# Kernel tuning notes

Measured on AMD Instinct MI355X. Metric: run time of the kernel, lower is better.

Reference implementation:

```python
import jax, jax.numpy as jnp
import numpy as np

N = 20000        # total atoms (atomic environments)
NFEAT = 2784     # power-spectrum feature size: sum_l n_max[l]^2 * n_pseudo^2
P = 4            # n_pseudo (alchemical pseudo-species)
H = 256          # MLP hidden width
S = 500          # number of structures
NSPEC = 8        # number of chemical species (len(all_species))
AVG_ATOMS = N / S  # average_number_of_atoms used for energy normalization


def setup_inputs() -> dict:
    key = jax.random.key(0)
    ks = jax.random.split(key, 8)
    features = jax.random.normal(ks[0], (N, NFEAT), dtype=jnp.float32)
    species = jax.random.randint(ks[1], (N,), 0, NSPEC)
    structure_idx = jax.random.randint(ks[2], (N,), 0, S)
    # combination matrix: Linear(n_species -> n_pseudo), no bias
    W_comb = jax.random.normal(ks[3], (NSPEC, P), dtype=jnp.float32) / np.float32(np.sqrt(NSPEC))
    # per-pseudo-species MLP weights (bias=False throughout)
    W1 = jax.random.normal(ks[4], (P, NFEAT, H), dtype=jnp.float32) / np.float32(np.sqrt(NFEAT))
    W2 = jax.random.normal(ks[5], (P, H, H), dtype=jnp.float32) / np.float32(np.sqrt(H))
    W3 = jax.random.normal(ks[6], (P, H, H), dtype=jnp.float32) / np.float32(np.sqrt(H))
    W4 = jax.random.normal(ks[7], (P, H, 1), dtype=jnp.float32) / np.float32(np.sqrt(H))
    return {"features": features, "W_comb": W_comb, "W1": W1, "W2": W2,
            "W3": W3, "W4": W4, "species": species, "structure_idx": structure_idx}


def reference(features, W_comb, W1, W2, W3, W4, species, structure_idx):
    # one-hot species encoding followed by combination_matrix linear map.
    # one_hot(species) @ W_comb  ==  W_comb[species]  (gather form, no [N, NSPEC] matmul)
    pseudo_w = W_comb[species]                                   # [N, P]
    # outer-product feature embedding: features[:, :, None] * pseudo_w[:, None, :]
    emb = features[:, :, None] * pseudo_w[:, None, :]            # [N, NFEAT, P]
    # per-pseudo-species MLP (Linear no-bias -> SiLU) x3 -> Linear to scalar,
    # vectorized over the pseudo dimension instead of a Python loop.
    h = jax.nn.silu(jnp.einsum('nfp,pfh->nph', emb, W1))         # [N, P, H]
    h = jax.nn.silu(jnp.einsum('nph,phk->npk', h, W2))           # [N, P, H]
    h = jax.nn.silu(jnp.einsum('nph,phk->npk', h, W3))           # [N, P, H]
    per_pseudo_e = jnp.einsum('nph,pho->npo', h, W4)[..., 0]     # [N, P]
    atomic_energies = per_pseudo_e.sum(axis=1) / np.float32(np.sqrt(P))  # [N]
    # scatter-add atomic energies into per-structure energies (index_add_)
    energies = jax.ops.segment_sum(atomic_energies, structure_idx, num_segments=S)
    return energies / np.float32(AVG_ATOMS)                     # [S]
```

## Files before the change

kernel.cpp:

```cpp
#include <hip/hip_runtime.h>
#include <hip/hip_bf16.h>
#include <stdint.h>

#define N_ATOMS 20000
#define NFEAT   2784
#define KP1     2816
#define KT1     44
#define SS      500
#define NPAD    20224
#define MCOLS   1024

typedef __attribute__((ext_vector_type(8))) short s16x8;
typedef __attribute__((ext_vector_type(4))) float f32x4;

static __device__ __forceinline__ unsigned short f2b(float f) {
    __hip_bfloat16 h = __float2bfloat16(f);
    return __builtin_bit_cast(unsigned short, h);
}
static __device__ __forceinline__ float b2f(unsigned short u) {
    unsigned int x = ((unsigned int)u) << 16;
    return __builtin_bit_cast(float, x);
}

#define GLOAD16(g, l) __builtin_amdgcn_global_load_lds( \
    (const __attribute__((address_space(1))) void*)(g), \
    (__attribute__((address_space(3))) void*)(l), 16, 0, 0)

__global__ void conv_feat(const float* __restrict__ F, unsigned short* __restrict__ out) {
    int row = blockIdx.x;
    int t = threadIdx.x;
    const float4* src = (const float4*)(F + (size_t)row * NFEAT);
    unsigned short* dst = out + (size_t)row * KP1;
    for (int g = t; g < KP1 / 4; g += 256) {
        float4 v;
        if (g < NFEAT / 4) v = src[g];
        else { v.x = 0.f; v.y = 0.f; v.z = 0.f; v.w = 0.f; }
        ushort4 o;
        o.x = f2b(v.x); o.y = f2b(v.y); o.z = f2b(v.z); o.w = f2b(v.w);
        *(ushort4*)(dst + g * 4) = o;
    }
}

__global__ void pack_w(const float* __restrict__ W, unsigned short* __restrict__ Bt,
                       int KD, int KP) {
    __shared__ unsigned short tile[32][256];
    int p = blockIdx.y;
    int f0 = blockIdx.x * 32;
    int t = threadIdx.x;
    #pragma unroll 4
    for (int i = 0; i < 32; ++i) {
        int f = f0 + i;
        float v = (f < KD) ? W[((size_t)p * KD + f) * 256 + t] : 0.f;
        tile[i][t] = f2b(v);
    }
    __syncthreads();
    unsigned short* drow = Bt + (size_t)(p * 256 + t) * KP + f0;
    #pragma unroll
    for (int i = 0; i < 32; i += 4) {
        ushort4 o;
        o.x = tile[i][t]; o.y = tile[i + 1][t]; o.z = tile[i + 2][t]; o.w = tile[i + 3][t];
        *(ushort4*)(drow + i) = o;
    }
}

__global__ void prep_small(const float* __restrict__ W2, const float* __restrict__ W3,
                           unsigned short* __restrict__ B2t, unsigned short* __restrict__ B3t,
                           const float* __restrict__ Wc, const int* __restrict__ spec,
                           float* __restrict__ pw, float* __restrict__ out) {
    __shared__ unsigned short tile[32][256];
    int b = blockIdx.x;
    int t = threadIdx.x;
    if (b < 64) {
        const float* W = (b < 32) ? W2 : W3;
        unsigned short* Bt = (b < 32) ? B2t : B3t;
        int bb = b & 31;
        int p = bb >> 3;
        int f0 = (bb & 7) * 32;
        #pragma unroll 4
        for (int i = 0; i < 32; ++i) {
            int f = f0 + i;
            tile[i][t] = f2b(W[((size_t)p * 256 + f) * 256 + t]);
        }
        __syncthreads();
        unsigned short* drow = Bt + (size_t)(p * 256 + t) * 256 + f0;
        #pragma unroll
        for (int i = 0; i < 32; i += 4) {
            ushort4 o;
            o.x = tile[i][t]; o.y = tile[i + 1][t]; o.z = tile[i + 2][t]; o.w = tile[i + 3][t];
            *(ushort4*)(drow + i) = o;
        }
    } else if (b < 143) {
        int n = (b - 64) * 256 + t;
        if (n < N_ATOMS) {
            int s = spec[n];
            float4 v = *(const float4*)(Wc + s * 4);
            *(float4*)(pw + n * 4) = v;
        }
    } else {
        for (int i = t; i < SS; i += 256) out[i] = 0.f;
    }
}

__global__ __launch_bounds__(512, 4) void gemm1_pipe(
    const unsigned short* __restrict__ A,
    const unsigned short* __restrict__ Bt,
    const float* __restrict__ pw,
    unsigned short* __restrict__ C)
{
    __shared__ __align__(16) unsigned short lds_a[2 * 8192];
    __shared__ __align__(16) unsigned short lds_b[2 * 8192];

    int bid = blockIdx.x;
    int swz = (bid & 7) * 158 + (bid >> 3);
    int rowTile = swz >> 3;
    int colTile = swz & 7;
    int rowBase = rowTile * 128;
    int colBase = colTile * 128;
    int p = colTile >> 1;

    int t0 = threadIdx.x;
    int wave = t0 >> 6;
    int lane = t0 & 63;
    int wm = wave >> 1;
    int wn = wave & 1;

    int rA = t0 >> 3;
    int ckl = ((t0 & 7) ^ (rA & 7)) << 3;
    const unsigned short* sa = A + (size_t)(rowBase + rA) * KP1 + ckl;
    const unsigned short* sb = Bt + (size_t)(colBase + rA) * KP1 + ckl;

    int ra0 = wm * 32 + (lane & 15);
    int rb0 = wn * 64 + (lane & 15);
    int xr = lane & 7;
    int c0 = lane >> 4;

    f32x4 acc[2][4];
    f32x4 z4 = {0.f, 0.f, 0.f, 0.f};
    #pragma unroll
    for (int i = 0; i < 2; ++i)
        #pragma unroll
        for (int j = 0; j < 4; ++j) acc[i][j] = z4;

#define STAGE1(SB) do { \
    GLOAD16(sa,                     lds_a + (SB) * 8192 + t0 * 8); \
    GLOAD16(sa + (size_t)64 * KP1,  lds_a + (SB) * 8192 + 4096 + t0 * 8); \
    GLOAD16(sb,                     lds_b + (SB) * 8192 + t0 * 8); \
    GLOAD16(sb + (size_t)64 * KP1,  lds_b + (SB) * 8192 + 4096 + t0 * 8); \
    sa += 64; sb += 64; \
} while (0)

    STAGE1(0);
    STAGE1(1);
    asm volatile("s_waitcnt vmcnt(4)" ::: "memory");
    __builtin_amdgcn_s_barrier();
    __builtin_amdgcn_sched_barrier(0);

#define FSTEP(CB) do { \
    s16x8 af[2][2], bv[2][4]; \
    _Pragma("unroll") \
    for (int kk = 0; kk < 2; ++kk) { \
        int ch = ((((kk << 2) | c0) ^ xr) << 3); \
        _Pragma("unroll") \
        for (int fm = 0; fm < 2; ++fm) \
            af[kk][fm] = *(const s16x8*)&lds_a[(CB) * 8192 + (ra0 + fm * 16) * 64 + ch]; \
        _Pragma("unroll") \
        for (int fn = 0; fn < 4; ++fn) \
            bv[kk][fn] = *(const s16x8*)&lds_b[(CB) * 8192 + (rb0 + fn * 16) * 64 + ch]; \
    } \
    asm volatile("s_waitcnt lgkmcnt(0)" ::: "memory"); \
    __builtin_amdgcn_sched_barrier(0); \
    __builtin_amdgcn_s_barrier();             \
    __builtin_amdgcn_sched_barrier(0); \
    STAGE1(CB);                               \
    __builtin_amdgcn_s_setprio(1); \
    _Pragma("unroll") \
    for (int kk = 0; kk < 2; ++kk) \
        _Pragma("unroll") \
        for (int fm = 0; fm < 2; ++fm) \
            _Pragma("unroll") \
            for (int fn = 0; fn < 4; ++fn) \
                acc[fm][fn] = __builtin_amdgcn_mfma_f32_16x16x32_bf16( \
                    af[kk][fm], bv[kk][fn], acc[fm][fn], 0, 0, 0); \
    __builtin_amdgcn_s_setprio(0); \
    asm volatile("s_waitcnt vmcnt(4)" ::: "memory");    \
    __builtin_amdgcn_s_barrier(); \
    __builtin_amdgcn_sched_barrier(0); \
} while (0)

#define TSTEP(CB, DRAIN) do { \
    s16x8 af[2][2], bv[2][4]; \
    _Pragma("unroll") \
    for (int kk = 0; kk < 2; ++kk) { \
        int ch = ((((kk << 2) | c0) ^ xr) << 3); \
        _Pragma("unroll") \
        for (int fm = 0; fm < 2; ++fm) \
            af[kk][fm] = *(const s16x8*)&lds_a[(CB) * 8192 + (ra0 + fm * 16) * 64 + ch]; \
        _Pragma("unroll") \
        for (int fn = 0; fn < 4; ++fn) \
            bv[kk][fn] = *(const s16x8*)&lds_b[(CB) * 8192 + (rb0 + fn * 16) * 64 + ch]; \
    } \
    _Pragma("unroll") \
    for (int kk = 0; kk < 2; ++kk) \
        _Pragma("unroll") \
        for (int fm = 0; fm < 2; ++fm) \
            _Pragma("unroll") \
            for (int fn = 0; fn < 4; ++fn) \
                acc[fm][fn] = __builtin_amdgcn_mfma_f32_16x16x32_bf16( \
                    af[kk][fm], bv[kk][fn], acc[fm][fn], 0, 0, 0); \
    if (DRAIN) { \
        asm volatile("s_waitcnt vmcnt(0)" ::: "memory"); \
        __builtin_amdgcn_s_barrier(); \
        __builtin_amdgcn_sched_barrier(0); \
    } \
} while (0)

    for (int it = 0; it < 21; ++it) {
        FSTEP(0);
        FSTEP(1);
    }
    TSTEP(0, 1);
    TSTEP(1, 0);
#undef FSTEP
#undef TSTEP
#undef STAGE1

    int rGrp = (lane >> 4) << 2;
    int cLane = lane & 15;
    #pragma unroll
    for (int fm = 0; fm < 2; ++fm) {
        int r0 = rowBase + wm * 32 + fm * 16 + rGrp;
        float pwv[4];
        #pragma unroll
        for (int j = 0; j < 4; ++j) pwv[j] = pw[(size_t)(r0 + j) * 4 + p];
        #pragma unroll
        for (int fn = 0; fn < 4; ++fn) {
            int c = colBase + wn * 64 + fn * 16 + cLane;
            f32x4 a = acc[fm][fn];
            #pragma unroll
            for (int j = 0; j < 4; ++j) {
                float x = a[j] * pwv[j];
                float s = x / (1.f + __expf(-x));
                C[(size_t)(r0 + j) * MCOLS + c] = f2b(s);
            }
        }
    }
}

template<int USE_PW>
__global__ __launch_bounds__(256, 2) void gemm_silu(
    const unsigned short* __restrict__ A, int lda,
    const unsigned short* __restrict__ Bt, int ldb,
    int K, int aOffPerP,
    const float* __restrict__ pw,
    unsigned short* __restrict__ C)
{
    __shared__ __align__(16) unsigned short lds_a[128 * 64];
    __shared__ __align__(16) unsigned short lds_b[128 * 64];

    int bid = blockIdx.x;
    int colTile = bid & 7;
    int rowTile = bid >> 3;
    int rowBase = rowTile * 128;
    int colBase = colTile * 128;
    int p = colBase >> 8;
    int aOff = p * aOffPerP;

    int t = threadIdx.x;
    int wave = t >> 6;
    int lane = t & 63;
    int wm = wave >> 1, wn = wave & 1;

    int trow = t >> 3;
    int kcol = (((t & 7) ^ (trow & 7)) << 3);
    const unsigned short* srcA = A + (size_t)(rowBase + trow) * lda + aOff + kcol;
    const unsigned short* srcB = Bt + (size_t)(colBase + trow) * ldb + kcol;

    f32x4 acc[4][4];
    f32x4 z4 = {0.f, 0.f, 0.f, 0.f};
    #pragma unroll
    for (int i = 0; i < 4; ++i)
        #pragma unroll
        for (int j = 0; j < 4; ++j) acc[i][j] = z4;

    int rb = wm * 64 + (lane & 15);
    int cb = wn * 64 + (lane & 15);
    int c0 = lane >> 4;
    int xr = lane & 7;

    int KT = K >> 6;
    for (int kt = 0; kt < KT; ++kt) {
        #pragma unroll
        for (int i = 0; i < 4; ++i) {
            GLOAD16(srcA + (size_t)i * 32 * lda, lds_a + i * 2048 + wave * 512);
            GLOAD16(srcB + (size_t)i * 32 * ldb, lds_b + i * 2048 + wave * 512);
        }
        srcA += 64; srcB += 64;
        __syncthreads();

        #pragma unroll
        for (int kk = 0; kk < 2; ++kk) {
            s16x8 af[4], bfr[4];
            int ch = (((kk << 2) | c0) ^ xr) << 3;
            #pragma unroll
            for (int fm = 0; fm < 4; ++fm)
                af[fm] = *(const s16x8*)&lds_a[(rb + fm * 16) * 64 + ch];
            #pragma unroll
            for (int fn = 0; fn < 4; ++fn)
                bfr[fn] = *(const s16x8*)&lds_b[(cb + fn * 16) * 64 + ch];
            #pragma unroll
            for (int fm = 0; fm < 4; ++fm)
                #pragma unroll
                for (int fn = 0; fn < 4; ++fn)
                    acc[fm][fn] = __builtin_amdgcn_mfma_f32_16x16x32_bf16(
                        af[fm], bfr[fn], acc[fm][fn], 0, 0, 0);
        }
        __syncthreads();
    }

    int rGrp = (lane >> 4) << 2;
    int cLane = lane & 15;
    #pragma unroll
    for (int fm = 0; fm < 4; ++fm) {
        int r0 = rowBase + wm * 64 + fm * 16 + rGrp;
        float pwv[4];
        if (USE_PW) {
            #pragma unroll
            for (int j = 0; j < 4; ++j) pwv[j] = pw[(size_t)(r0 + j) * 4 + p];
        }
        #pragma unroll
        for (int fn = 0; fn < 4; ++fn) {
            int c = colBase + wn * 64 + fn * 16 + cLane;
            f32x4 a = acc[fm][fn];
            #pragma unroll
            for (int j = 0; j < 4; ++j) {
                float x = a[j];
                if (USE_PW) x *= pwv[j];
                float s = x / (1.f + __expf(-x));
                C[(size_t)(r0 + j) * MCOLS + c] = f2b(s);
            }
        }
    }
}

__global__ void finalize(const unsigned short* __restrict__ h3,
                         const float* __restrict__ W4,
                         const int* __restrict__ sidx,
                         float* __restrict__ out) {
    int atom = blockIdx.x * 4 + (threadIdx.x >> 6);
    int lane = threadIdx.x & 63;
    if (atom >= N_ATOMS) return;
    const uint32_t* hu = (const uint32_t*)(h3 + (size_t)atom * MCOLS) + lane * 8;
    const float* w = W4 + lane * 16;
    float sum = 0.f;
    #pragma unroll
    for (int i = 0; i < 8; ++i) {
        uint32_t u = hu[i];
        sum += b2f((unsigned short)(u & 0xffff)) * w[2 * i];
        sum += b2f((unsigned short)(u >> 16)) * w[2 * i + 1];
    }
    #pragma unroll
    for (int off = 32; off > 0; off >>= 1) sum += __shfl_down(sum, off);
    if (lane == 0) atomicAdd(out + sidx[atom], sum * 0.0125f);
}

extern "C" void kernel_launch(void* const* d_in, const int* in_sizes, int n_in,
                              void* d_out, int out_size, void* d_ws, size_t ws_size,
                              hipStream_t stream) {
    const float* features = (const float*)d_in[0];
    const float* W_comb   = (const float*)d_in[1];
    const float* W1       = (const float*)d_in[2];
    const float* W2       = (const float*)d_in[3];
    const float* W3       = (const float*)d_in[4];
    const float* W4       = (const float*)d_in[5];
    const int*   species  = (const int*)d_in[6];
    const int*   sidx     = (const int*)d_in[7];
    float* out = (float*)d_out;

    char* ws = (char*)d_ws;
    size_t off = 0;
    auto carve = [&](size_t bytes) {
        char* r = ws + off;
        off += (bytes + 255) & ~(size_t)255;
        return r;
    };
    unsigned short* feat = (unsigned short*)carve((size_t)NPAD * KP1 * 2);
    unsigned short* B1t  = (unsigned short*)carve((size_t)1024 * KP1 * 2 + 4096);
    unsigned short* B2t  = (unsigned short*)carve((size_t)1024 * 256 * 2);
    unsigned short* B3t  = (unsigned short*)carve((size_t)1024 * 256 * 2);
    float*          pw   = (float*)carve((size_t)NPAD * 4 * 4);
    unsigned short* h1   = (unsigned short*)carve((size_t)NPAD * 1024 * 2);
    carve(4096);
    unsigned short* h2   = feat;

    conv_feat<<<N_ATOMS, 256, 0, stream>>>(features, feat);
    pack_w<<<dim3(KP1 / 32, 4), 256, 0, stream>>>(W1, B1t, NFEAT, KP1);
    prep_small<<<144, 256, 0, stream>>>(W2, W3, B2t, B3t, W_comb, species, pw, out);

    gemm1_pipe<<<158 * 8, 512, 0, stream>>>(feat, B1t, pw, h1);
    gemm_silu<0><<<158 * 8, 256, 0, stream>>>(h1, 1024, B2t, 256, 256, 256, nullptr, h2);
    gemm_silu<0><<<158 * 8, 256, 0, stream>>>(h2, 1024, B3t, 256, 256, 256, nullptr, h1);
    finalize<<<N_ATOMS / 4, 256, 0, stream>>>(h1, W4, sidx, out);
}
```

Measured before the change: 284.9 us.

## Fuse fp32-to-bf16 feature conversion into GEMM1 A-tile loading

```diff
diff --git a/kernel.cpp b/kernel.cpp
--- a/kernel.cpp
+++ b/kernel.cpp
@@ -5,7 +5,6 @@
 #define N_ATOMS 20000
 #define NFEAT   2784
 #define KP1     2816
-#define KT1     44
 #define SS      500
 #define NPAD    20224
 #define MCOLS   1024
@@ -25,21 +24,6 @@
 #define GLOAD16(g, l) __builtin_amdgcn_global_load_lds( \
     (const __attribute__((address_space(1))) void*)(g), \
     (__attribute__((address_space(3))) void*)(l), 16, 0, 0)
-
-__global__ void conv_feat(const float* __restrict__ F, unsigned short* __restrict__ out) {
-    int row = blockIdx.x;
-    int t = threadIdx.x;
-    const float4* src = (const float4*)(F + (size_t)row * NFEAT);
-    unsigned short* dst = out + (size_t)row * KP1;
-    for (int g = t; g < KP1 / 4; g += 256) {
-        float4 v;
-        if (g < NFEAT / 4) v = src[g];
-        else { v.x = 0.f; v.y = 0.f; v.z = 0.f; v.w = 0.f; }
-        ushort4 o;
-        o.x = f2b(v.x); o.y = f2b(v.y); o.z = f2b(v.z); o.w = f2b(v.w);
-        *(ushort4*)(dst + g * 4) = o;
-    }
-}
 
 __global__ void pack_w(const float* __restrict__ W, unsigned short* __restrict__ Bt,
                        int KD, int KP) {
@@ -101,8 +85,8 @@
     }
 }
 
-__global__ __launch_bounds__(512, 4) void gemm1_pipe(
-    const unsigned short* __restrict__ A,
+__global__ __launch_bounds__(512, 4) void gemm1_fused(
+    const float* __restrict__ F,
     const unsigned short* __restrict__ Bt,
     const float* __restrict__ pw,
     unsigned short* __restrict__ C)
@@ -125,9 +109,17 @@
     int wn = wave & 1;
 
     int rA = t0 >> 3;
-    int ckl = ((t0 & 7) ^ (rA & 7)) << 3;
-    const unsigned short* sa = A + (size_t)(rowBase + rA) * KP1 + ckl;
-    const unsigned short* sb = Bt + (size_t)(colBase + rA) * KP1 + ckl;
+    int cl = t0 & 7;
+    int cl8 = cl << 3;
+    int pc = cl ^ (rA & 7);
+    int ar0 = rowBase + rA;      if (ar0 > N_ATOMS - 1) ar0 = N_ATOMS - 1;
+    int ar1 = rowBase + rA + 64; if (ar1 > N_ATOMS - 1) ar1 = N_ATOMS - 1;
+    const float* fa0 = F + (size_t)ar0 * NFEAT;
+    const float* fa1 = F + (size_t)ar1 * NFEAT;
+    unsigned short* wA0 = lds_a + rA * 64 + pc * 8;
+    unsigned short* wA1 = lds_a + (rA + 64) * 64 + pc * 8;
+
+    const unsigned short* sb = Bt + (size_t)(colBase + rA) * KP1 + (pc << 3);
 
     int ra0 = wm * 32 + (lane & 15);
     int rb0 = wn * 64 + (lane & 15);
@@ -141,21 +133,57 @@
         #pragma unroll
         for (int j = 0; j < 4; ++j) acc[i][j] = z4;
 
-#define STAGE1(SB) do { \
-    GLOAD16(sa,                     lds_a + (SB) * 8192 + t0 * 8); \
-    GLOAD16(sa + (size_t)64 * KP1,  lds_a + (SB) * 8192 + 4096 + t0 * 8); \
-    GLOAD16(sb,                     lds_b + (SB) * 8192 + t0 * 8); \
-    GLOAD16(sb + (size_t)64 * KP1,  lds_b + (SB) * 8192 + 4096 + t0 * 8); \
-    sa += 64; sb += 64; \
+#define AISSUE(KO, R0_, R1_, R2_, R3_) do { \
+    int ko = (KO) + cl8; if (ko > NFEAT - 8) ko = NFEAT - 8; \
+    R0_ = *(const float4*)(fa0 + ko); \
+    R1_ = *(const float4*)(fa0 + ko + 4); \
+    R2_ = *(const float4*)(fa1 + ko); \
+    R3_ = *(const float4*)(fa1 + ko + 4); \
 } while (0)
 
-    STAGE1(0);
-    STAGE1(1);
-    asm volatile("s_waitcnt vmcnt(4)" ::: "memory");
+#define AWRITE(SB, C0, C1, C2, C3) do { \
+    s16x8 w0, w1; \
+    w0[0] = (short)f2b((C0).x); w0[1] = (short)f2b((C0).y); \
+    w0[2] = (short)f2b((C0).z); w0[3] = (short)f2b((C0).w); \
+    w0[4] = (short)f2b((C1).x); w0[5] = (short)f2b((C1).y); \
+    w0[6] = (short)f2b((C1).z); w0[7] = (short)f2b((C1).w); \
+    w1[0] = (short)f2b((C2).x); w1[1] = (short)f2b((C2).y); \
+    w1[2] = (short)f2b((C2).z); w1[3] = (short)f2b((C2).w); \
+    w1[4] = (short)f2b((C3).x); w1[5] = (short)f2b((C3).y); \
+    w1[6] = (short)f2b((C3).z); w1[7] = (short)f2b((C3).w); \
+    *(s16x8*)(wA0 + (SB) * 8192) = w0; \
+    *(s16x8*)(wA1 + (SB) * 8192) = w1; \
+} while (0)
+
+#define BGLOAD(SB) do { \
+    GLOAD16(sb, lds_b + (SB) * 8192 + t0 * 8); \
+    GLOAD16(sb + (size_t)64 * KP1, lds_b + (SB) * 8192 + 4096 + t0 * 8); \
+    sb += 64; \
+} while (0)
+
+    float4 a00, a01, a02, a03;
+    float4 a10, a11, a12, a13;
+    AISSUE(0,   a00, a01, a02, a03);
+    __builtin_amdgcn_sched_barrier(0);
+    AISSUE(64,  a10, a11, a12, a13);
+    __builtin_amdgcn_sched_barrier(0);
+    BGLOAD(0);
+    BGLOAD(1);
+    asm volatile("s_waitcnt vmcnt(8)" ::: "memory");
+    AWRITE(0, a00, a01, a02, a03);
+    AISSUE(128, a00, a01, a02, a03);
+    __builtin_amdgcn_sched_barrier(0);
+    asm volatile("s_waitcnt vmcnt(8)" ::: "memory");
+    AWRITE(1, a10, a11, a12, a13);
+    AISSUE(192, a10, a11, a12, a13);
+    __builtin_amdgcn_sched_barrier(0);
+    asm volatile("s_waitcnt vmcnt(10) lgkmcnt(0)" ::: "memory");
     __builtin_amdgcn_s_barrier();
     __builtin_amdgcn_sched_barrier(0);
 
-#define FSTEP(CB) do { \
+    int ako = 256;
+
+#define FSTEP(CB, C0, C1, C2, C3) do { \
     s16x8 af[2][2], bv[2][4]; \
     _Pragma("unroll") \
     for (int kk = 0; kk < 2; ++kk) { \
@@ -171,7 +199,11 @@
     __builtin_amdgcn_sched_barrier(0); \
     __builtin_amdgcn_s_barrier();             \
     __builtin_amdgcn_sched_barrier(0); \
-    STAGE1(CB);                               \
+    AWRITE(CB, C0, C1, C2, C3);               \
+    AISSUE(ako, C0, C1, C2, C3);              \
+    ako += 64; \
+    __builtin_amdgcn_sched_barrier(0); \
+    BGLOAD(CB);                               \
     __builtin_amdgcn_s_setprio(1); \
     _Pragma("unroll") \
     for (int kk = 0; kk < 2; ++kk) \
@@ -182,47 +214,21 @@
                 acc[fm][fn] = __builtin_amdgcn_mfma_f32_16x16x32_bf16( \
                     af[kk][fm], bv[kk][fn], acc[fm][fn], 0, 0, 0); \
     __builtin_amdgcn_s_setprio(0); \
-    asm volatile("s_waitcnt vmcnt(4)" ::: "memory");    \
+    asm volatile("s_waitcnt vmcnt(6) lgkmcnt(0)" ::: "memory");  \
     __builtin_amdgcn_s_barrier(); \
     __builtin_amdgcn_sched_barrier(0); \
 } while (0)
 
-#define TSTEP(CB, DRAIN) do { \
-    s16x8 af[2][2], bv[2][4]; \
-    _Pragma("unroll") \
-    for (int kk = 0; kk < 2; ++kk) { \
-        int ch = ((((kk << 2) | c0) ^ xr) << 3); \
-        _Pragma("unroll") \
-        for (int fm = 0; fm < 2; ++fm) \
-            af[kk][fm] = *(const s16x8*)&lds_a[(CB) * 8192 + (ra0 + fm * 16) * 64 + ch]; \
-        _Pragma("unroll") \
-        for (int fn = 0; fn < 4; ++fn) \
-            bv[kk][fn] = *(const s16x8*)&lds_b[(CB) * 8192 + (rb0 + fn * 16) * 64 + ch]; \
-    } \
-    _Pragma("unroll") \
-    for (int kk = 0; kk < 2; ++kk) \
-        _Pragma("unroll") \
-        for (int fm = 0; fm < 2; ++fm) \
-            _Pragma("unroll") \
-            for (int fn = 0; fn < 4; ++fn) \
-                acc[fm][fn] = __builtin_amdgcn_mfma_f32_16x16x32_bf16( \
-                    af[kk][fm], bv[kk][fn], acc[fm][fn], 0, 0, 0); \
-    if (DRAIN) { \
-        asm volatile("s_waitcnt vmcnt(0)" ::: "memory"); \
-        __builtin_amdgcn_s_barrier(); \
-        __builtin_amdgcn_sched_barrier(0); \
-    } \
-} while (0)
-
-    for (int it = 0; it < 21; ++it) {
-        FSTEP(0);
-        FSTEP(1);
-    }
-    TSTEP(0, 1);
-    TSTEP(1, 0);
+    for (int it = 0; it < 22; ++it) {
+        FSTEP(0, a00, a01, a02, a03);
+        FSTEP(1, a10, a11, a12, a13);
+    }
 #undef FSTEP
-#undef TSTEP
-#undef STAGE1
+#undef BGLOAD
+#undef AWRITE
+#undef AISSUE
+
+    asm volatile("s_waitcnt vmcnt(0) lgkmcnt(0)" ::: "memory");
 
     int rGrp = (lane >> 4) << 2;
     int cLane = lane & 15;
@@ -383,20 +389,18 @@
         off += (bytes + 255) & ~(size_t)255;
         return r;
     };
-    unsigned short* feat = (unsigned short*)carve((size_t)NPAD * KP1 * 2);
     unsigned short* B1t  = (unsigned short*)carve((size_t)1024 * KP1 * 2 + 4096);
     unsigned short* B2t  = (unsigned short*)carve((size_t)1024 * 256 * 2);
     unsigned short* B3t  = (unsigned short*)carve((size_t)1024 * 256 * 2);
     float*          pw   = (float*)carve((size_t)NPAD * 4 * 4);
     unsigned short* h1   = (unsigned short*)carve((size_t)NPAD * 1024 * 2);
+    unsigned short* h2   = (unsigned short*)carve((size_t)NPAD * 1024 * 2);
     carve(4096);
-    unsigned short* h2   = feat;
-
-    conv_feat<<<N_ATOMS, 256, 0, stream>>>(features, feat);
+
     pack_w<<<dim3(KP1 / 32, 4), 256, 0, stream>>>(W1, B1t, NFEAT, KP1);
     prep_small<<<144, 256, 0, stream>>>(W2, W3, B2t, B3t, W_comb, species, pw, out);
 
-    gemm1_pipe<<<158 * 8, 512, 0, stream>>>(feat, B1t, pw, h1);
+    gemm1_fused<<<158 * 8, 512, 0, stream>>>(features, B1t, pw, h1);
     gemm_silu<0><<<158 * 8, 256, 0, stream>>>(h1, 1024, B2t, 256, 256, 256, nullptr, h2);
     gemm_silu<0><<<158 * 8, 256, 0, stream>>>(h2, 1024, B3t, 256, 256, 256, nullptr, h1);
     finalize<<<N_ATOMS / 4, 256, 0, stream>>>(h1, W4, sidx, out);
```

Result: slower. 476.1 us (+67.1%).

## Fuse layer-3 GEMM with W4 dot product and merge prep kernels

Applied to the files above, without the earlier changes.

```diff
diff --git a/kernel.cpp b/kernel.cpp
--- a/kernel.cpp
+++ b/kernel.cpp
@@ -5,7 +5,6 @@
 #define N_ATOMS 20000
 #define NFEAT   2784
 #define KP1     2816
-#define KT1     44
 #define SS      500
 #define NPAD    20224
 #define MCOLS   1024
@@ -26,78 +25,75 @@
     (const __attribute__((address_space(1))) void*)(g), \
     (__attribute__((address_space(3))) void*)(l), 16, 0, 0)
 
-__global__ void conv_feat(const float* __restrict__ F, unsigned short* __restrict__ out) {
-    int row = blockIdx.x;
-    int t = threadIdx.x;
-    const float4* src = (const float4*)(F + (size_t)row * NFEAT);
-    unsigned short* dst = out + (size_t)row * KP1;
-    for (int g = t; g < KP1 / 4; g += 256) {
-        float4 v;
-        if (g < NFEAT / 4) v = src[g];
-        else { v.x = 0.f; v.y = 0.f; v.z = 0.f; v.w = 0.f; }
-        ushort4 o;
-        o.x = f2b(v.x); o.y = f2b(v.y); o.z = f2b(v.z); o.w = f2b(v.w);
-        *(ushort4*)(dst + g * 4) = o;
-    }
-}
-
-__global__ void pack_w(const float* __restrict__ W, unsigned short* __restrict__ Bt,
-                       int KD, int KP) {
-    __shared__ unsigned short tile[32][256];
-    int p = blockIdx.y;
-    int f0 = blockIdx.x * 32;
-    int t = threadIdx.x;
-    #pragma unroll 4
-    for (int i = 0; i < 32; ++i) {
-        int f = f0 + i;
-        float v = (f < KD) ? W[((size_t)p * KD + f) * 256 + t] : 0.f;
-        tile[i][t] = f2b(v);
-    }
-    __syncthreads();
-    unsigned short* drow = Bt + (size_t)(p * 256 + t) * KP + f0;
-    #pragma unroll
-    for (int i = 0; i < 32; i += 4) {
-        ushort4 o;
-        o.x = tile[i][t]; o.y = tile[i + 1][t]; o.z = tile[i + 2][t]; o.w = tile[i + 3][t];
-        *(ushort4*)(drow + i) = o;
-    }
-}
-
-__global__ void prep_small(const float* __restrict__ W2, const float* __restrict__ W3,
-                           unsigned short* __restrict__ B2t, unsigned short* __restrict__ B3t,
-                           const float* __restrict__ Wc, const int* __restrict__ spec,
-                           float* __restrict__ pw, float* __restrict__ out) {
+__global__ void prep_all(const float* __restrict__ F, unsigned short* __restrict__ feat,
+                         const float* __restrict__ W1, unsigned short* __restrict__ B1t,
+                         const float* __restrict__ W2, const float* __restrict__ W3,
+                         unsigned short* __restrict__ B2t, unsigned short* __restrict__ B3t,
+                         const float* __restrict__ Wc, const int* __restrict__ spec,
+                         float* __restrict__ pw, float* __restrict__ out) {
     __shared__ unsigned short tile[32][256];
     int b = blockIdx.x;
     int t = threadIdx.x;
-    if (b < 64) {
-        const float* W = (b < 32) ? W2 : W3;
-        unsigned short* Bt = (b < 32) ? B2t : B3t;
-        int bb = b & 31;
-        int p = bb >> 3;
-        int f0 = (bb & 7) * 32;
+    if (b < N_ATOMS) {
+        const float4* src = (const float4*)(F + (size_t)b * NFEAT);
+        unsigned short* dst = feat + (size_t)b * KP1;
+        for (int g = t; g < KP1 / 4; g += 256) {
+            float4 v;
+            if (g < NFEAT / 4) v = src[g];
+            else { v.x = 0.f; v.y = 0.f; v.z = 0.f; v.w = 0.f; }
+            ushort4 o;
+            o.x = f2b(v.x); o.y = f2b(v.y); o.z = f2b(v.z); o.w = f2b(v.w);
+            *(ushort4*)(dst + g * 4) = o;
+        }
+    } else if (b < N_ATOMS + 352) {
+        int bb = b - N_ATOMS;
+        int p = bb / 88;
+        int f0 = (bb % 88) * 32;
         #pragma unroll 4
         for (int i = 0; i < 32; ++i) {
             int f = f0 + i;
-            tile[i][t] = f2b(W[((size_t)p * 256 + f) * 256 + t]);
+            float v = (f < NFEAT) ? W1[((size_t)p * NFEAT + f) * 256 + t] : 0.f;
+            tile[i][t] = f2b(v);
         }
         __syncthreads();
-        unsigned short* drow = Bt + (size_t)(p * 256 + t) * 256 + f0;
+        unsigned short* drow = B1t + (size_t)(p * 256 + t) * KP1 + f0;
         #pragma unroll
         for (int i = 0; i < 32; i += 4) {
             ushort4 o;
             o.x = tile[i][t]; o.y = tile[i + 1][t]; o.z = tile[i + 2][t]; o.w = tile[i + 3][t];
             *(ushort4*)(drow + i) = o;
         }
-    } else if (b < 143) {
-        int n = (b - 64) * 256 + t;
-        if (n < N_ATOMS) {
-            int s = spec[n];
-            float4 v = *(const float4*)(Wc + s * 4);
-            *(float4*)(pw + n * 4) = v;
-        }
     } else {
-        for (int i = t; i < SS; i += 256) out[i] = 0.f;
+        int bb = b - N_ATOMS - 352;
+        if (bb < 64) {
+            const float* W = (bb < 32) ? W2 : W3;
+            unsigned short* Bt = (bb < 32) ? B2t : B3t;
+            int b2 = bb & 31;
+            int p = b2 >> 3;
+            int f0 = (b2 & 7) * 32;
+            #pragma unroll 4
+            for (int i = 0; i < 32; ++i) {
+                int f = f0 + i;
+                tile[i][t] = f2b(W[((size_t)p * 256 + f) * 256 + t]);
+            }
+            __syncthreads();
+            unsigned short* drow = Bt + (size_t)(p * 256 + t) * 256 + f0;
+            #pragma unroll
+            for (int i = 0; i < 32; i += 4) {
+                ushort4 o;
+                o.x = tile[i][t]; o.y = tile[i + 1][t]; o.z = tile[i + 2][t]; o.w = tile[i + 3][t];
+                *(ushort4*)(drow + i) = o;
+            }
+        } else if (bb < 143) {
+            int n = (bb - 64) * 256 + t;
+            if (n < N_ATOMS) {
+                int s = spec[n];
+                float4 v = *(const float4*)(Wc + s * 4);
+                *(float4*)(pw + n * 4) = v;
+            }
+        } else {
+            for (int i = t; i < SS; i += 256) out[i] = 0.f;
+        }
     }
 }
 
@@ -342,25 +338,111 @@
     }
 }
 
-__global__ void finalize(const unsigned short* __restrict__ h3,
-                         const float* __restrict__ W4,
-                         const int* __restrict__ sidx,
-                         float* __restrict__ out) {
-    int atom = blockIdx.x * 4 + (threadIdx.x >> 6);
-    int lane = threadIdx.x & 63;
-    if (atom >= N_ATOMS) return;
-    const uint32_t* hu = (const uint32_t*)(h3 + (size_t)atom * MCOLS) + lane * 8;
-    const float* w = W4 + lane * 16;
-    float sum = 0.f;
-    #pragma unroll
-    for (int i = 0; i < 8; ++i) {
-        uint32_t u = hu[i];
-        sum += b2f((unsigned short)(u & 0xffff)) * w[2 * i];
-        sum += b2f((unsigned short)(u >> 16)) * w[2 * i + 1];
-    }
-    #pragma unroll
-    for (int off = 32; off > 0; off >>= 1) sum += __shfl_down(sum, off);
-    if (lane == 0) atomicAdd(out + sidx[atom], sum * 0.0125f);
+__global__ __launch_bounds__(256, 2) void gemm_dot3(
+    const unsigned short* __restrict__ A,
+    const unsigned short* __restrict__ Bt,
+    const float* __restrict__ W4,
+    float* __restrict__ ep)
+{
+    __shared__ __align__(16) unsigned short lds_a[128 * 64];
+    __shared__ __align__(16) unsigned short lds_b[128 * 64];
+
+    int bid = blockIdx.x;
+    int colTile = bid & 7;
+    int rowTile = bid >> 3;
+    int rowBase = rowTile * 128;
+    int colBase = colTile * 128;
+    int p = colBase >> 8;
+    int aOff = p * 256;
+
+    int t = threadIdx.x;
+    int wave = t >> 6;
+    int lane = t & 63;
+    int wm = wave >> 1, wn = wave & 1;
+
+    int trow = t >> 3;
+    int kcol = (((t & 7) ^ (trow & 7)) << 3);
+    const unsigned short* srcA = A + (size_t)(rowBase + trow) * 1024 + aOff + kcol;
+    const unsigned short* srcB = Bt + (size_t)(colBase + trow) * 256 + kcol;
+
+    f32x4 acc[4][4];
+    f32x4 z4 = {0.f, 0.f, 0.f, 0.f};
+    #pragma unroll
+    for (int i = 0; i < 4; ++i)
+        #pragma unroll
+        for (int j = 0; j < 4; ++j) acc[i][j] = z4;
+
+    int rb = wm * 64 + (lane & 15);
+    int cb = wn * 64 + (lane & 15);
+    int c0 = lane >> 4;
+    int xr = lane & 7;
+
+    for (int kt = 0; kt < 4; ++kt) {
+        #pragma unroll
+        for (int i = 0; i < 4; ++i) {
+            GLOAD16(srcA + (size_t)i * 32 * 1024, lds_a + i * 2048 + wave * 512);
+            GLOAD16(srcB + (size_t)i * 32 * 256,  lds_b + i * 2048 + wave * 512);
+        }
+        srcA += 64; srcB += 64;
+        __syncthreads();
+
+        #pragma unroll
+        for (int kk = 0; kk < 2; ++kk) {
+            s16x8 af[4], bfr[4];
+            int ch = (((kk << 2) | c0) ^ xr) << 3;
+            #pragma unroll
+            for (int fm = 0; fm < 4; ++fm)
+                af[fm] = *(const s16x8*)&lds_a[(rb + fm * 16) * 64 + ch];
+            #pragma unroll
+            for (int fn = 0; fn < 4; ++fn)
+                bfr[fn] = *(const s16x8*)&lds_b[(cb + fn * 16) * 64 + ch];
+            #pragma unroll
+            for (int fm = 0; fm < 4; ++fm)
+                #pragma unroll
+                for (int fn = 0; fn < 4; ++fn)
+                    acc[fm][fn] = __builtin_amdgcn_mfma_f32_16x16x32_bf16(
+                        af[fm], bfr[fn], acc[fm][fn], 0, 0, 0);
+        }
+        __syncthreads();
+    }
+
+    int rGrp = (lane >> 4) << 2;
+    int cLane = lane & 15;
+    float w4v[4];
+    #pragma unroll
+    for (int fn = 0; fn < 4; ++fn)
+        w4v[fn] = W4[colBase + wn * 64 + fn * 16 + cLane];
+    #pragma unroll
+    for (int fm = 0; fm < 4; ++fm) {
+        #pragma unroll
+        for (int j = 0; j < 4; ++j) {
+            float s = 0.f;
+            #pragma unroll
+            for (int fn = 0; fn < 4; ++fn) {
+                float x = acc[fm][fn][j];
+                s += (x / (1.f + __expf(-x))) * w4v[fn];
+            }
+            s += __shfl_xor(s, 1);
+            s += __shfl_xor(s, 2);
+            s += __shfl_xor(s, 4);
+            s += __shfl_xor(s, 8);
+            if (cLane == 0) {
+                int row = rowBase + wm * 64 + fm * 16 + rGrp + j;
+                ep[(size_t)row * 16 + colTile * 2 + wn] = s;
+            }
+        }
+    }
+}
+
+__global__ void finalize2(const float* __restrict__ ep, const int* __restrict__ sidx,
+                          float* __restrict__ out) {
+    int n = blockIdx.x * 256 + threadIdx.x;
+    if (n >= N_ATOMS) return;
+    const float4* v = (const float4*)(ep + (size_t)n * 16);
+    float4 a = v[0], b = v[1], c = v[2], d = v[3];
+    float s = (a.x + a.y + a.z + a.w) + (b.x + b.y + b.z + b.w)
+            + (c.x + c.y + c.z + c.w) + (d.x + d.y + d.z + d.w);
+    atomicAdd(out + sidx[n], s * 0.0125f);
 }
 
 extern "C" void kernel_launch(void* const* d_in, const int* in_sizes, int n_in,
@@ -389,15 +471,15 @@
     unsigned short* B3t  = (unsigned short*)carve((size_t)1024 * 256 * 2);
     float*          pw   = (float*)carve((size_t)NPAD * 4 * 4);
     unsigned short* h1   = (unsigned short*)carve((size_t)NPAD * 1024 * 2);
+    float*          ep   = (float*)carve((size_t)NPAD * 16 * 4);
     carve(4096);
     unsigned short* h2   = feat;
 
-    conv_feat<<<N_ATOMS, 256, 0, stream>>>(features, feat);
-    pack_w<<<dim3(KP1 / 32, 4), 256, 0, stream>>>(W1, B1t, NFEAT, KP1);
-    prep_small<<<144, 256, 0, stream>>>(W2, W3, B2t, B3t, W_comb, species, pw, out);
+    prep_all<<<N_ATOMS + 352 + 144, 256, 0, stream>>>(
+        features, feat, W1, B1t, W2, W3, B2t, B3t, W_comb, species, pw, out);
 
     gemm1_pipe<<<158 * 8, 512, 0, stream>>>(feat, B1t, pw, h1);
     gemm_silu<0><<<158 * 8, 256, 0, stream>>>(h1, 1024, B2t, 256, 256, 256, nullptr, h2);
-    gemm_silu<0><<<158 * 8, 256, 0, stream>>>(h2, 1024, B3t, 256, 256, 256, nullptr, h1);
-    finalize<<<N_ATOMS / 4, 256, 0, stream>>>(h1, W4, sidx, out);
-}
+    gemm_dot3<<<158 * 8, 256, 0, stream>>>(h2, B3t, W4, ep);
+    finalize2<<<(N_ATOMS + 255) / 256, 256, 0, stream>>>(ep, sidx, out);
+}
```

Result: faster. 265.6 us (median of 2 runs) (-6.8%).
